# Kernel tuning notes

Hardware: AMD Instinct MI355X
Metric: run time of the kernel (lower is better)

The kernel has to match this reference:

```python
import jax, jax.numpy as jnp
import numpy as np

B = 16384   # batch of feature vectors
D = 1024    # backbone.hidden_dim
T = 20      # n_tasks
C = 100     # num_classes // n_tasks = n_classes_per_head


def setup_inputs() -> dict:
    key = jax.random.key(0)
    k1, k2, k3, k4 = jax.random.split(key, 4)
    x = jax.random.normal(k1, (B, D), dtype=jnp.float32)
    t = jax.random.randint(k2, (B,), 0, T)  # per-sample task id in [0, T)
    # Stacked per-task Linear params (PyTorch Linear: y = x @ W.T + b, W is [C, D])
    W = jax.random.normal(k3, (T, C, D), dtype=jnp.float32) * (1.0 / np.sqrt(D))
    b = jax.random.normal(k4, (T, C), dtype=jnp.float32) * 0.01
    return {"x": x, "t": t, "W": W, "b": b}


def reference(x, t, W, b):
    """Faithful vectorization of forward_head.

    Original: for each unique task, gather rows with t==task, apply that
    task's Linear, scatter results back into pred. Equivalent math:
    pred[i] = W[t[i]] @ x[i] + b[t[i]].

    We compute all T heads in one dense einsum ([B,T,C] = 131MB, cheap vs a
    [B,C,D] gathered-weight tensor) and select each sample's own task row.
    """
    logits_all = jnp.einsum('bd,tcd->btc', x, W) + b[None, :, :]  # [B, T, C]
    pred = jnp.take_along_axis(logits_all, t[:, None, None], axis=1)[:, 0, :]  # [B, C]
    return pred
```

## Files before the change

kernel.cpp:

```cpp
#include <hip/hip_runtime.h>
#include <hip/hip_bf16.h>

#define NB 16384
#define ND 1024
#define NT 20
#define NC 100
#define NTILES_MAX 532
#define STEPS 16
#define ABUF 8192
#define BBUF 14336
#define BUFB (ABUF + BBUF)

typedef __bf16  bf16x8 __attribute__((ext_vector_type(8)));
typedef float   f32x4  __attribute__((ext_vector_type(4)));
typedef unsigned short ushort_t;

__device__ __forceinline__ unsigned int f2bf(float f) {
    unsigned int u = __builtin_bit_cast(unsigned int, f);
    u += 0x7FFFu + ((u >> 16) & 1u);
    return u >> 16;
}
__device__ __forceinline__ unsigned long long pack4(float a, float b, float c, float d) {
    return (unsigned long long)f2bf(a)
         | ((unsigned long long)f2bf(b) << 16)
         | ((unsigned long long)f2bf(c) << 32)
         | ((unsigned long long)f2bf(d) << 48);
}
__device__ __forceinline__ bf16x8 mk_frag(float4 a, float4 b) {
    union { unsigned long long u[2]; bf16x8 v; } r;
    r.u[0] = pack4(a.x, a.y, a.z, a.w);
    r.u[1] = pack4(b.x, b.y, b.z, b.w);
    return r.v;
}

__device__ __forceinline__ void async_cp16(const void* g, void* l) {
    auto gp = reinterpret_cast<const __attribute__((address_space(1))) unsigned int*>(
        reinterpret_cast<unsigned long long>(g));
    auto lp = reinterpret_cast<__attribute__((address_space(3))) unsigned int*>(
        static_cast<unsigned int>(reinterpret_cast<unsigned long long>(l)));
    __builtin_amdgcn_global_load_lds(gp, lp, 16, 0, 0);
}


__global__ void bucket_kernel(const int* __restrict__ t, int* __restrict__ offsets,
                              int* __restrict__ tiles, int* __restrict__ idx_list) {
    __shared__ int h[NT], off[NT + 1], cur[NT], tb[NT + 1];
    const int tid = threadIdx.x;
    if (tid < NT) h[tid] = 0;
    __syncthreads();
    const int4* t4 = (const int4*)t;
    int4 v[4];
#pragma unroll
    for (int k = 0; k < 4; ++k) v[k] = t4[tid + k * 1024];
#pragma unroll
    for (int k = 0; k < 4; ++k) {
        atomicAdd(&h[v[k].x], 1); atomicAdd(&h[v[k].y], 1);
        atomicAdd(&h[v[k].z], 1); atomicAdd(&h[v[k].w], 1);
    }
    __syncthreads();
    if (tid == 0) {
        int acc = 0, tv = 0;
        for (int i = 0; i < NT; ++i) {
            off[i] = acc; cur[i] = acc; tb[i] = tv;
            acc += h[i]; tv += (h[i] + 31) >> 5;
        }
        off[NT] = acc; tb[NT] = tv;
    }
    __syncthreads();
    if (tid <= NT) offsets[tid] = off[tid];
    const int ntiles = tb[NT];
    for (int g = tid; g < NTILES_MAX; g += 1024) {
        int e = -1;
        if (g < ntiles) {
            int task = 0;
            while (tb[task + 1] <= g) ++task;
            e = (task << 16) | (g - tb[task]);
        }
        tiles[g] = e;
    }
#pragma unroll
    for (int k = 0; k < 4; ++k) {
        int base = (tid + k * 1024) * 4;
        idx_list[atomicAdd(&cur[v[k].x], 1)] = base;
        idx_list[atomicAdd(&cur[v[k].y], 1)] = base + 1;
        idx_list[atomicAdd(&cur[v[k].z], 1)] = base + 2;
        idx_list[atomicAdd(&cur[v[k].w], 1)] = base + 3;
    }
}


__global__ void wcvt_kernel(const float* __restrict__ W, ushort_t* __restrict__ Wf) {
    int g = blockIdx.x * 256 + threadIdx.x;
    int kg   = g & 127;
    int rest = g >> 7;
    int c    = rest % 112;
    int task = rest / 112;
    unsigned long long u0 = 0, u1 = 0;
    if (c < NC) {
        const float* p = W + ((size_t)(task * NC + c)) * ND + kg * 8;
        float4 a = *(const float4*)p;
        float4 b = *(const float4*)(p + 4);
        u0 = pack4(a.x, a.y, a.z, a.w);
        u1 = pack4(b.x, b.y, b.z, b.w);
    }
    size_t dst = (((size_t)task * 32 + (kg >> 2)) * 7 + (c >> 4)) * 512
               + (size_t)((c & 15) | ((kg & 3) << 4)) * 8;
    *(unsigned long long*)(Wf + dst)     = u0;
    *(unsigned long long*)(Wf + dst + 4) = u1;
}


__global__ __launch_bounds__(256, 3) void gemm_kernel(
    const float* __restrict__ x, const ushort_t* __restrict__ Wfrag,
    const float* __restrict__ bias, const int* __restrict__ offsets,
    const int* __restrict__ tiles, const int* __restrict__ idx_list,
    float* __restrict__ out)
{
    __shared__ __align__(16) char lds[2 * BUFB];
    const int ent = tiles[blockIdx.x];
    if (ent < 0) return;
    const int task = ent >> 16;
    const int m0   = (ent & 0xffff) << 5;
    const int seg  = offsets[task];
    const int cnt  = offsets[task + 1] - seg;

    const int tid  = threadIdx.x;
    const int wid  = tid >> 6;
    const int lane = tid & 63;
    const int wm   = wid >> 1;
    const int wn   = wid & 1;
    const int csel = lane & 15;
    const int q    = lane >> 4;

    const float* srcA[2];
#pragma unroll
    for (int jj = 0; jj < 2; ++jj) {
        int j    = 2 * wid + jj;
        int row  = j * 4 + q;
        int byte = csel * 16;
        int logb = byte ^ ((row & 7) << 4);
        int sr   = m0 + row; if (sr > cnt - 1) sr = cnt - 1;
        srcA[jj] = x + (size_t)idx_list[seg + sr] * ND + (logb >> 2);
    }
    const ushort_t* srcB = Wfrag + (size_t)task * (32 * 7 * 512) + lane * 8;
    int bii[4];
#pragma unroll
    for (int jj = 0; jj < 4; ++jj) {
        int i = wid + 4 * jj;
        bii[jj] = (i < 14) ? i : (i - 14);
    }

    auto STAGE = [&](int s) {
        char* Ab = lds + (s & 1) * BUFB;
        char* Bb = Ab + ABUF;
        async_cp16(srcA[0] + s * 64, Ab + (2 * wid + 0) * 1024);
        async_cp16(srcA[1] + s * 64, Ab + (2 * wid + 1) * 1024);
#pragma unroll
        for (int jj = 0; jj < 4; ++jj)
            async_cp16(srcB + (size_t)(s * 14 + bii[jj]) * 512, Bb + bii[jj] * 1024);
    };

    const int rowA = wm * 16 + csel;
    const unsigned swzA = (unsigned)((rowA & 7) << 4);
    const int nfr = wn ? 3 : 4;
    f32x4 acc[4] = {};

    auto COMPUTE = [&](int s) {
        const char* Ab = lds + (s & 1) * BUFB;
        const char* Bb = Ab + ABUF;
        const char* Ar = Ab + rowA * 256;
#pragma unroll
        for (int kkb = 0; kkb < 2; ++kkb) {
            unsigned abase = (unsigned)(kkb * 128 + q * 32);
            float4 a0 = *(const float4*)(Ar + (abase ^ swzA));
            float4 a1 = *(const float4*)(Ar + ((abase + 16) ^ swzA));
            bf16x8 af = mk_frag(a0, a1);
#pragma unroll
            for (int nf = 0; nf < 4; ++nf) {
                if (nf < nfr) {
                    int f = wn * 4 + nf;
                    bf16x8 bf = *(const bf16x8*)(Bb + (kkb * 7 + f) * 1024 + lane * 16);
                    acc[nf] = __builtin_amdgcn_mfma_f32_16x16x32_bf16(af, bf, acc[nf], 0, 0, 0);
                }
            }
        }
    };

    STAGE(0);
    STAGE(1);
    asm volatile("s_waitcnt vmcnt(6)" ::: "memory");
    __builtin_amdgcn_sched_barrier(0);
    __builtin_amdgcn_s_barrier();

#pragma unroll 1
    for (int s = 0; s < STEPS; ++s) {
        COMPUTE(s);
        if (s == STEPS - 1) break;
        asm volatile("s_waitcnt lgkmcnt(0)" ::: "memory");
        __builtin_amdgcn_s_barrier();
        if (s < STEPS - 2) {
            STAGE(s + 2);
            asm volatile("s_waitcnt vmcnt(6)" ::: "memory");
        } else {
            asm volatile("s_waitcnt vmcnt(0)" ::: "memory");
        }
        __builtin_amdgcn_sched_barrier(0);
        __builtin_amdgcn_s_barrier();
    }

    int oi[4];
#pragma unroll
    for (int rr = 0; rr < 4; ++rr) {
        int gm = m0 + wm * 16 + q * 4 + rr;
        oi[rr] = (gm < cnt) ? idx_list[seg + gm] : -1;
    }
#pragma unroll
    for (int nf = 0; nf < 4; ++nf) {
        if (nf < nfr) {
            int cg = (wn * 4 + nf) * 16 + csel;
            if (cg < NC) {
                float bv = bias[task * NC + cg];
#pragma unroll
                for (int rr = 0; rr < 4; ++rr)
                    if (oi[rr] >= 0)
                        out[(size_t)oi[rr] * NC + cg] = acc[nf][rr] + bv;
            }
        }
    }
}


extern "C" void kernel_launch(void* const* d_in, const int* in_sizes, int n_in,
                              void* d_out, int out_size, void* d_ws, size_t ws_size,
                              hipStream_t stream) {
    const float* x    = (const float*)d_in[0];
    const int*   t    = (const int*)d_in[1];
    const float* W    = (const float*)d_in[2];
    const float* bias = (const float*)d_in[3];

    char* ws = (char*)d_ws;
    int* offsets  = (int*)ws;
    int* tiles    = (int*)(ws + 128);
    int* idx_list = (int*)(ws + 4352);
    ushort_t* Wf  = (ushort_t*)(ws + 69888);

    wcvt_kernel  <<<20 * 112 * 128 / 256, 256, 0, stream>>>(W, Wf);
    bucket_kernel<<<1, 1024, 0, stream>>>(t, offsets, tiles, idx_list);
    gemm_kernel  <<<NTILES_MAX, 256, 0, stream>>>(x, Wf, bias, offsets, tiles,
                                                  idx_list, (float*)d_out);
}
```

Baseline: 41.69 us.

## Merge weight-convert and bucketing kernels; triple-buffer GEMM LDS pipeline

Fuses the weight bf16 conversion and task bucketing into one prep kernel launch, with block 280 doing the bucketing, which drops one launch and lets both jobs run at once. Separately, the GEMM moves from a double-buffered to a triple-buffered async global-to-LDS pipeline with a prefetch depth of three stages and matching vmcnt waits. The extra buffer raises LDS use per block, so launch bounds drop to 2 blocks per SM, trading occupancy for deeper latency hiding.

```diff
diff --git a/kernel.cpp b/kernel.cpp
--- a/kernel.cpp
+++ b/kernel.cpp
@@ -42,10 +42,33 @@
 }
 
 
-__global__ void bucket_kernel(const int* __restrict__ t, int* __restrict__ offsets,
-                              int* __restrict__ tiles, int* __restrict__ idx_list) {
+__global__ __launch_bounds__(1024) void prep_kernel(
+    const float* __restrict__ W, ushort_t* __restrict__ Wf,
+    const int* __restrict__ t, int* __restrict__ offsets,
+    int* __restrict__ tiles, int* __restrict__ idx_list)
+{
+    const int tid = threadIdx.x;
+    if (blockIdx.x < 280) {
+        int g = blockIdx.x * 1024 + tid;
+        int kg   = g & 127;
+        int rest = g >> 7;
+        int c    = rest % 112;
+        int task = rest / 112;
+        unsigned long long u0 = 0, u1 = 0;
+        if (c < NC) {
+            const float* p = W + ((size_t)(task * NC + c)) * ND + kg * 8;
+            float4 a = *(const float4*)p;
+            float4 b = *(const float4*)(p + 4);
+            u0 = pack4(a.x, a.y, a.z, a.w);
+            u1 = pack4(b.x, b.y, b.z, b.w);
+        }
+        size_t dst = (((size_t)task * 32 + (kg >> 2)) * 7 + (c >> 4)) * 512
+                   + (size_t)((c & 15) | ((kg & 3) << 4)) * 8;
+        *(unsigned long long*)(Wf + dst)     = u0;
+        *(unsigned long long*)(Wf + dst + 4) = u1;
+        return;
+    }
     __shared__ int h[NT], off[NT + 1], cur[NT], tb[NT + 1];
-    const int tid = threadIdx.x;
     if (tid < NT) h[tid] = 0;
     __syncthreads();
     const int4* t4 = (const int4*)t;
@@ -89,34 +112,13 @@
 }
 
 
-__global__ void wcvt_kernel(const float* __restrict__ W, ushort_t* __restrict__ Wf) {
-    int g = blockIdx.x * 256 + threadIdx.x;
-    int kg   = g & 127;
-    int rest = g >> 7;
-    int c    = rest % 112;
-    int task = rest / 112;
-    unsigned long long u0 = 0, u1 = 0;
-    if (c < NC) {
-        const float* p = W + ((size_t)(task * NC + c)) * ND + kg * 8;
-        float4 a = *(const float4*)p;
-        float4 b = *(const float4*)(p + 4);
-        u0 = pack4(a.x, a.y, a.z, a.w);
-        u1 = pack4(b.x, b.y, b.z, b.w);
-    }
-    size_t dst = (((size_t)task * 32 + (kg >> 2)) * 7 + (c >> 4)) * 512
-               + (size_t)((c & 15) | ((kg & 3) << 4)) * 8;
-    *(unsigned long long*)(Wf + dst)     = u0;
-    *(unsigned long long*)(Wf + dst + 4) = u1;
-}
-
-
-__global__ __launch_bounds__(256, 3) void gemm_kernel(
+__global__ __launch_bounds__(256, 2) void gemm_kernel(
     const float* __restrict__ x, const ushort_t* __restrict__ Wfrag,
     const float* __restrict__ bias, const int* __restrict__ offsets,
     const int* __restrict__ tiles, const int* __restrict__ idx_list,
     float* __restrict__ out)
 {
-    __shared__ __align__(16) char lds[2 * BUFB];
+    __shared__ __align__(16) char lds[3 * BUFB];
     const int ent = tiles[blockIdx.x];
     if (ent < 0) return;
     const int task = ent >> 16;
@@ -150,8 +152,7 @@
         bii[jj] = (i < 14) ? i : (i - 14);
     }
 
-    auto STAGE = [&](int s) {
-        char* Ab = lds + (s & 1) * BUFB;
+    auto STAGE = [&](int s, char* Ab) {
         char* Bb = Ab + ABUF;
         async_cp16(srcA[0] + s * 64, Ab + (2 * wid + 0) * 1024);
         async_cp16(srcA[1] + s * 64, Ab + (2 * wid + 1) * 1024);
@@ -165,8 +166,7 @@
     const int nfr = wn ? 3 : 4;
     f32x4 acc[4] = {};
 
-    auto COMPUTE = [&](int s) {
-        const char* Ab = lds + (s & 1) * BUFB;
+    auto COMPUTE = [&](const char* Ab) {
         const char* Bb = Ab + ABUF;
         const char* Ar = Ab + rowA * 256;
 #pragma unroll
@@ -186,26 +186,32 @@
         }
     };
 
-    STAGE(0);
-    STAGE(1);
-    asm volatile("s_waitcnt vmcnt(6)" ::: "memory");
+    STAGE(0, lds);
+    STAGE(1, lds + BUFB);
+    STAGE(2, lds + 2 * BUFB);
+    asm volatile("s_waitcnt vmcnt(12)" ::: "memory");
     __builtin_amdgcn_sched_barrier(0);
     __builtin_amdgcn_s_barrier();
 
+    int bufc = 0;
 #pragma unroll 1
     for (int s = 0; s < STEPS; ++s) {
-        COMPUTE(s);
+        char* Ab = lds + bufc * BUFB;
+        COMPUTE(Ab);
         if (s == STEPS - 1) break;
         asm volatile("s_waitcnt lgkmcnt(0)" ::: "memory");
         __builtin_amdgcn_s_barrier();
-        if (s < STEPS - 2) {
-            STAGE(s + 2);
+        if (s < STEPS - 3) {
+            STAGE(s + 3, Ab);
+            asm volatile("s_waitcnt vmcnt(12)" ::: "memory");
+        } else if (s == STEPS - 3) {
             asm volatile("s_waitcnt vmcnt(6)" ::: "memory");
         } else {
             asm volatile("s_waitcnt vmcnt(0)" ::: "memory");
         }
         __builtin_amdgcn_sched_barrier(0);
         __builtin_amdgcn_s_barrier();
+        bufc = (bufc == 2) ? 0 : bufc + 1;
     }
 
     int oi[4];
@@ -244,8 +250,7 @@
     int* idx_list = (int*)(ws + 4352);
     ushort_t* Wf  = (ushort_t*)(ws + 69888);
 
-    wcvt_kernel  <<<20 * 112 * 128 / 256, 256, 0, stream>>>(W, Wf);
-    bucket_kernel<<<1, 1024, 0, stream>>>(t, offsets, tiles, idx_list);
-    gemm_kernel  <<<NTILES_MAX, 256, 0, stream>>>(x, Wf, bias, offsets, tiles,
-                                                  idx_list, (float*)d_out);
-}
+    prep_kernel<<<281, 1024, 0, stream>>>(W, Wf, t, offsets, tiles, idx_list);
+    gemm_kernel<<<NTILES_MAX, 256, 0, stream>>>(x, Wf, bias, offsets, tiles,
+                                                idx_list, (float*)d_out);
+}
```

After: 52.21 us. +25.2%, slower.
